# Kernel tuning notes

Measured on AMD Instinct MI355X. Metric: run time of the kernel, lower is better.

The kernel has to match this reference:

```python
import jax, jax.numpy as jnp
import numpy as np

MASK_NEG = 1e30


def setup_inputs() -> dict:
    key = jax.random.key(0)
    k_q, k_k, k_m, k_w1, k_w2, k_v = jax.random.split(key, 6)
    B, S, D, A = 32, 2048, 1024, 1024  # batch, seq, feature dim, attn dim
    # Xavier-uniform-like scale for weights
    lim = float(np.sqrt(6.0 / (D + A)))
    query = jax.random.normal(k_q, (B, D), dtype=jnp.float32)
    keys = jax.random.normal(k_k, (B, S, D), dtype=jnp.float32)
    mask = jax.random.randint(k_m, (B, S), 0, 2) > 0  # True = keep
    W1 = jax.random.uniform(k_w1, (A, D), jnp.float32, -lim, lim)
    W2 = jax.random.uniform(k_w2, (A, D), jnp.float32, -lim, lim)
    v = jax.random.uniform(k_v, (A,), jnp.float32, -lim, lim)
    return {"query": query, "keys": keys, "mask": mask, "W1": W1, "W2": W2, "v": v}


def reference(query, keys, mask, W1, W2, v):
    w1_query = jnp.einsum('bd,ad->ba', query, W1)          # (B, A)
    w2_keys = jnp.einsum('bsd,ad->bsa', keys, W2)          # (B, S, A)
    combined = jnp.tanh(w1_query[:, None, :] + w2_keys)    # (B, S, A)
    scores = jnp.einsum('bsa,a->bs', combined, v)          # (B, S)
    # masked softmax: subtract huge constant at masked-out positions
    scores = scores - (~mask).astype(scores.dtype) * MASK_NEG
    return jax.nn.softmax(scores, axis=-1)
```

## Files before the change

kernel.cpp:

```cpp
#include <hip/hip_runtime.h>
#include <hip/hip_bf16.h>
#include <stdint.h>

#define NB 32
#define NS 2048
#define ND 1024
#define NA 1024
#define MASK_NEG 1e30f

#define BM 256
#define BN 256
#define BK 64
#define NTILES 64

typedef __attribute__((ext_vector_type(4))) float f32x4;
typedef __attribute__((ext_vector_type(8))) __bf16 bf16x8;

__device__ __forceinline__ void glds16(const void* g, void* l) {
  __builtin_amdgcn_global_load_lds(
      (const __attribute__((address_space(1))) uint32_t*)g,
      (__attribute__((address_space(3))) uint32_t*)(uintptr_t)l, 16, 0, 0);
}

__global__ void zero_f32(float* __restrict__ p, int n) {
  int i = blockIdx.x * 256 + threadIdx.x;
  if (i < n) p[i] = 0.f;
}

__global__ __launch_bounds__(256) void cvt_bf16(const float* __restrict__ in,
                                                __bf16* __restrict__ out, int n8) {
  long i = blockIdx.x * 256 + threadIdx.x;
  const long stride = (long)gridDim.x * 256;
  for (; i < n8; i += stride) {
    f32x4 a = ((const f32x4*)in)[2 * i];
    f32x4 b = ((const f32x4*)in)[2 * i + 1];
    bf16x8 o;
#pragma unroll
    for (int j = 0; j < 4; ++j) { o[j] = (__bf16)a[j]; o[4 + j] = (__bf16)b[j]; }
    ((bf16x8*)out)[i] = o;
  }
}

__global__ __launch_bounds__(256) void w1q_kernel(const float* __restrict__ q,
                                                  const float* __restrict__ W1,
                                                  float* __restrict__ w1q) {
  const int b = blockIdx.x;
  const int a0 = blockIdx.y * 64;
  const int t = threadIdx.x;
  const int al = t >> 2;
  const int part = t & 3;
  const float* wrow = W1 + (size_t)(a0 + al) * ND + part * 256;
  const float* qrow = q + (size_t)b * ND + part * 256;
  float sum = 0.f;
#pragma unroll 8
  for (int i = 0; i < 256; i += 4) {
    float4 w = *reinterpret_cast<const float4*>(wrow + i);
    float4 x = *reinterpret_cast<const float4*>(qrow + i);
    sum += w.x * x.x + w.y * x.y + w.z * x.z + w.w * x.w;
  }
  __shared__ float red[256];
  red[t] = sum;
  __syncthreads();
  if (t < 64) {
    w1q[(size_t)b * NA + a0 + t] = red[t * 4] + red[t * 4 + 1] + red[t * 4 + 2] + red[t * 4 + 3];
  }
}

__global__ __launch_bounds__(512, 1) void score_gemm8(
    const __bf16* __restrict__ keysb, const __bf16* __restrict__ W2b,
    const float* __restrict__ w1q, const float* __restrict__ vvec,
    float* __restrict__ scores) {
  __shared__ __bf16 ldsA[6][128 * BK];
  __shared__ __bf16 ldsB[4][128 * BK];

  const int t = threadIdx.x;
  const int bs0 = blockIdx.x * BM;
  const int b = bs0 >> 11;
  const int lane = t & 63;
  const int wid = t >> 6;
  const int wr = wid >> 2;
  const int wc = wid & 3;
  const int lrow = lane & 15;
  const int ko = lane >> 4;

  const int srow = lane >> 3;
  const int scol = (lane & 7) ^ srow;
  const size_t aoffT = (size_t)(bs0 + wid * 16 + srow) * ND + scol * 8;
  const size_t boffT = (size_t)(wid * 16 + srow) * ND + scol * 8;

  const int sl0 = ko ^ (lrow & 7);
  const int sl1 = (4 + ko) ^ (lrow & 7);

#define STAGE_A(T, H)                                                           \
  do {                                                                          \
    if ((T) < NTILES) {                                                         \
      const unsigned slot_ = (2u * (unsigned)(T) + (unsigned)(H)) % 6u;         \
      char* d_ = (char*)ldsA + (slot_ << 14) + wid * 2048;                      \
      const size_t g_ = aoffT + (size_t)((H)*128) * ND + (size_t)(((T)&15) * BK); \
      glds16(keysb + g_, d_);                                                   \
      glds16(keysb + g_ + (size_t)8 * ND, d_ + 1024);                           \
    }                                                                           \
  } while (0)

#define STAGE_B(T, H)                                                           \
  do {                                                                          \
    if ((T) < NTILES) {                                                         \
      const unsigned slot_ = (2u * (unsigned)(T) + (unsigned)(H)) % 4u;         \
      char* d_ = (char*)ldsB + (slot_ << 14) + wid * 2048;                      \
      const size_t g_ = boffT + (size_t)(((T) >> 4) * 256 + (H)*128) * ND +     \
                        (size_t)(((T)&15) * BK);                                \
      glds16(W2b + g_, d_);                                                     \
      glds16(W2b + g_ + (size_t)8 * ND, d_ + 1024);                             \
    }                                                                           \
  } while (0)

#define SB __builtin_amdgcn_sched_barrier(0)
#define P1 __builtin_amdgcn_s_setprio(1)
#define P0 __builtin_amdgcn_s_setprio(0)
#define BAR __builtin_amdgcn_s_barrier()

#define PHASE(TL, M_, N_, STAGE_STMT, WM)                                       \
  do {                                                                          \
    STAGE_STMT;                                                                 \
    if ((N_) == 0) {                                                            \
      const char* Ab_ =                                                         \
          (const char*)ldsA + (((2u * (unsigned)(TL) + (unsigned)wr) % 6u) << 14); \
      _Pragma("unroll") for (int mi = 0; mi < 4; ++mi) {                        \
        const int ra_ = (((M_)*4 + mi) * 16 + lrow) * 128;                      \
        af[mi][0] = *reinterpret_cast<const bf16x8*>(Ab_ + ra_ + sl0 * 16);     \
        af[mi][1] = *reinterpret_cast<const bf16x8*>(Ab_ + ra_ + sl1 * 16);     \
      }                                                                         \
    }                                                                           \
    {                                                                           \
      const char* Bb_ =                                                         \
          (const char*)ldsB + (((2u * (unsigned)(TL) + (unsigned)(wc >> 1)) % 4u) << 14); \
      _Pragma("unroll") for (int nq = 0; nq < 2; ++nq) {                        \
        const int rb_ = (((wc & 1) * 4 + (N_)*2 + nq) * 16 + lrow) * 128;       \
        bfr[nq][0] = *reinterpret_cast<const bf16x8*>(Bb_ + rb_ + sl0 * 16);    \
        bfr[nq][1] = *reinterpret_cast<const bf16x8*>(Bb_ + rb_ + sl1 * 16);    \
      }                                                                         \
    }                                                                           \
    BAR;                                                                        \
    asm volatile("s_waitcnt lgkmcnt(0)");                                       \
    SB;                                                                         \
    P1;                                                                         \
    _Pragma("unroll") for (int mi = 0; mi < 4; ++mi)                            \
        _Pragma("unroll") for (int nq = 0; nq < 2; ++nq) {                      \
      acc[(M_)*4 + mi][(N_)*2 + nq] = __builtin_amdgcn_mfma_f32_16x16x32_bf16(  \
          af[mi][0], bfr[nq][0], acc[(M_)*4 + mi][(N_)*2 + nq], 0, 0, 0);       \
      acc[(M_)*4 + mi][(N_)*2 + nq] = __builtin_amdgcn_mfma_f32_16x16x32_bf16(  \
          af[mi][1], bfr[nq][1], acc[(M_)*4 + mi][(N_)*2 + nq], 0, 0, 0);       \
    }                                                                           \
    P0;                                                                         \
    if (WM) {                                                                   \
      if (it != 31) { asm volatile("s_waitcnt vmcnt(4)"); }                     \
      else { asm volatile("s_waitcnt vmcnt(0)"); }                              \
      SB;                                                                       \
    }                                                                           \
    BAR;                                                                        \
  } while (0)

  f32x4 acc[8][4];
#pragma unroll
  for (int mi = 0; mi < 8; ++mi)
#pragma unroll
    for (int ni = 0; ni < 4; ++ni) acc[mi][ni] = f32x4{0.f, 0.f, 0.f, 0.f};

  bf16x8 af[4][2], bfr[2][2];

  STAGE_A(0, 0);
  STAGE_A(0, 1);
  STAGE_A(1, 0);
  STAGE_A(1, 1);
  STAGE_B(0, 0);
  STAGE_B(0, 1);
  __syncthreads();

  for (int it = 0; it < 32; ++it) {
    const int t0 = 2 * it, t1 = 2 * it + 1;
    PHASE(t0, 0, 0, STAGE_B(t1, 0), 0);
    PHASE(t0, 0, 1, STAGE_B(t1, 1), 0);
    PHASE(t0, 1, 0, STAGE_A(t0 + 2, 0), 0);
    PHASE(t0, 1, 1, STAGE_A(t0 + 2, 1), 1);
    PHASE(t1, 0, 0, STAGE_B(t0 + 2, 0), 0);
    PHASE(t1, 0, 1, { STAGE_B(t0 + 2, 1); STAGE_A(t1 + 2, 0); }, 0);
    PHASE(t1, 1, 0, STAGE_A(t1 + 2, 1), 0);
    PHASE(t1, 1, 1, {}, 1);

    if ((it & 7) == 7) {
      const int a0 = (it >> 3) * BN;
      float w1v[4], vv[4];
#pragma unroll
      for (int ni = 0; ni < 4; ++ni) {
        const int a = a0 + wc * 64 + ni * 16 + lrow;
        w1v[ni] = w1q[(size_t)b * NA + a];
        vv[ni] = vvec[a];
      }
#pragma unroll
      for (int mi = 0; mi < 8; ++mi)
#pragma unroll
        for (int r = 0; r < 4; ++r) {
          float p = 0.f;
#pragma unroll
          for (int ni = 0; ni < 4; ++ni) {
            const float x = acc[mi][ni][r] + w1v[ni];
            const float e = __expf(2.f * x);
            p += (1.f - 2.f * __builtin_amdgcn_rcpf(e + 1.f)) * vv[ni];
          }
          p += __shfl_xor(p, 1);
          p += __shfl_xor(p, 2);
          p += __shfl_xor(p, 4);
          p += __shfl_xor(p, 8);
          if (lrow == 0)
            atomicAdd(&scores[bs0 + wr * 128 + mi * 16 + ko * 4 + r], p);
        }
#pragma unroll
      for (int mi = 0; mi < 8; ++mi)
#pragma unroll
        for (int ni = 0; ni < 4; ++ni) acc[mi][ni] = f32x4{0.f, 0.f, 0.f, 0.f};
    }
  }

#undef STAGE_A
#undef STAGE_B
#undef PHASE
#undef SB
#undef P1
#undef P0
#undef BAR
}

__global__ __launch_bounds__(256) void softmax_kernel(const float* __restrict__ scores,
                                                      const int* __restrict__ mask,
                                                      float* __restrict__ out) {
  const int b = blockIdx.x;
  const int t = threadIdx.x;
  float sc[8];
  float mx = -3.4e38f;
#pragma unroll
  for (int j = 0; j < 8; ++j) {
    int i = t + j * 256;
    float s = scores[b * NS + i];
    if (mask[b * NS + i] == 0) s -= MASK_NEG;
    sc[j] = s;
    mx = fmaxf(mx, s);
  }
#pragma unroll
  for (int off = 1; off < 64; off <<= 1) mx = fmaxf(mx, __shfl_xor(mx, off));
  __shared__ float redm[4];
  __shared__ float reds[4];
  if ((t & 63) == 0) redm[t >> 6] = mx;
  __syncthreads();
  mx = fmaxf(fmaxf(redm[0], redm[1]), fmaxf(redm[2], redm[3]));
  float e[8];
  float sum = 0.f;
#pragma unroll
  for (int j = 0; j < 8; ++j) {
    e[j] = __expf(sc[j] - mx);
    sum += e[j];
  }
#pragma unroll
  for (int off = 1; off < 64; off <<= 1) sum += __shfl_xor(sum, off);
  if ((t & 63) == 0) reds[t >> 6] = sum;
  __syncthreads();
  sum = reds[0] + reds[1] + reds[2] + reds[3];
  float inv = 1.f / sum;
#pragma unroll
  for (int j = 0; j < 8; ++j) out[b * NS + t + j * 256] = e[j] * inv;
}

extern "C" void kernel_launch(void* const* d_in, const int* in_sizes, int n_in,
                              void* d_out, int out_size, void* d_ws, size_t ws_size,
                              hipStream_t stream) {
  const float* q = (const float*)d_in[0];
  const float* keysf = (const float*)d_in[1];
  const int* mask = (const int*)d_in[2];
  const float* W1 = (const float*)d_in[3];
  const float* W2f = (const float*)d_in[4];
  const float* v = (const float*)d_in[5];
  float* out = (float*)d_out;

  float* scores = (float*)d_ws;
  float* w1q = scores + NB * NS;
  __bf16* W2b = (__bf16*)(w1q + NB * NA);
  __bf16* keysb = (__bf16*)((char*)W2b + (size_t)NA * ND * 2);

  zero_f32<<<NB * NS / 256, 256, 0, stream>>>(scores, NB * NS);
  cvt_bf16<<<512, 256, 0, stream>>>(W2f, W2b, NA * ND / 8);
  cvt_bf16<<<2048, 256, 0, stream>>>(keysf, keysb, (int)((size_t)NB * NS * ND / 8));
  w1q_kernel<<<dim3(NB, NA / 64), 256, 0, stream>>>(q, W1, w1q);
  score_gemm8<<<NB * NS / BM, 512, 0, stream>>>(keysb, W2b, w1q, v, scores);
  softmax_kernel<<<NB, 256, 0, stream>>>(scores, mask, out);
}
```

Measured before the change: 257.5 us.

## Fuse keys fp32-to-bf16 conversion into score GEMM first pass

Removes the separate keys conversion kernel. During the first A-column block the GEMM loads fp32 keys into registers, converts them to bf16, writes them to LDS and also stores the bf16 copy to global. Later column blocks then read that copy with direct-to-LDS loads. This avoids a full extra write-and-read pass over keys, but the first 16 tiles now use a register path with full vmcnt waits, which may stall the pipeline there.

```diff
diff --git a/kernel.cpp b/kernel.cpp
--- a/kernel.cpp
+++ b/kernel.cpp
@@ -67,7 +67,8 @@
 }
 
 __global__ __launch_bounds__(512, 1) void score_gemm8(
-    const __bf16* __restrict__ keysb, const __bf16* __restrict__ W2b,
+    const float* __restrict__ keysf, __bf16* __restrict__ keysb,
+    const __bf16* __restrict__ W2b,
     const float* __restrict__ w1q, const float* __restrict__ vvec,
     float* __restrict__ scores) {
   __shared__ __bf16 ldsA[6][128 * BK];
@@ -85,28 +86,56 @@
 
   const int srow = lane >> 3;
   const int scol = (lane & 7) ^ srow;
-  const size_t aoffT = (size_t)(bs0 + wid * 16 + srow) * ND + scol * 8;
   const size_t boffT = (size_t)(wid * 16 + srow) * ND + scol * 8;
 
   const int sl0 = ko ^ (lrow & 7);
   const int sl1 = (4 + ko) ^ (lrow & 7);
 
-#define STAGE_A(T, H)                                                           \
+  f32x4 la[4];
+
+#define ALOAD(T, H)                                                             \
+  do {                                                                          \
+    if ((T) < 16) {                                                             \
+      const float* gp_ = keysf +                                                \
+          (size_t)(bs0 + (H)*128 + wid * 16 + srow) * ND + ((T)&15) * 64 + scol * 8; \
+      la[0] = *reinterpret_cast<const f32x4*>(gp_);                             \
+      la[1] = *reinterpret_cast<const f32x4*>(gp_ + 4);                         \
+      la[2] = *reinterpret_cast<const f32x4*>(gp_ + (size_t)8 * ND);            \
+      la[3] = *reinterpret_cast<const f32x4*>(gp_ + (size_t)8 * ND + 4);        \
+    }                                                                           \
+  } while (0)
+
+#define AWRITE(T, H)                                                            \
   do {                                                                          \
     if ((T) < NTILES) {                                                         \
-      const unsigned slot_ = (2u * (unsigned)(T) + (unsigned)(H)) % 6u;         \
-      char* d_ = (char*)ldsA + (slot_ << 14) + wid * 2048;                      \
-      const size_t g_ = aoffT + (size_t)((H)*128) * ND + (size_t)(((T)&15) * BK); \
-      glds16(keysb + g_, d_);                                                   \
-      glds16(keysb + g_ + (size_t)8 * ND, d_ + 1024);                           \
+      char* du_ = (char*)ldsA + (((2u * (unsigned)(T) + (unsigned)(H)) % 6u) << 14) + \
+                  wid * 2048;                                                   \
+      if ((T) < 16) {                                                           \
+        bf16x8 o0_, o1_;                                                        \
+        _Pragma("unroll") for (int j = 0; j < 4; ++j) {                         \
+          o0_[j] = (__bf16)la[0][j]; o0_[4 + j] = (__bf16)la[1][j];             \
+          o1_[j] = (__bf16)la[2][j]; o1_[4 + j] = (__bf16)la[3][j];             \
+        }                                                                       \
+        *reinterpret_cast<bf16x8*>(du_ + lane * 16) = o0_;                      \
+        *reinterpret_cast<bf16x8*>(du_ + 1024 + lane * 16) = o1_;               \
+        __bf16* gs_ = keysb +                                                   \
+            (size_t)(bs0 + (H)*128 + wid * 16 + srow) * ND + ((T)&15) * 64 + scol * 8; \
+        *reinterpret_cast<bf16x8*>(gs_) = o0_;                                  \
+        *reinterpret_cast<bf16x8*>(gs_ + (size_t)8 * ND) = o1_;                 \
+      } else {                                                                  \
+        const size_t g_ = (size_t)(bs0 + (H)*128 + wid * 16 + srow) * ND +      \
+                          ((T)&15) * 64 + scol * 8;                             \
+        glds16(keysb + g_, du_);                                                \
+        glds16(keysb + g_ + (size_t)8 * ND, du_ + 1024);                        \
+      }                                                                         \
     }                                                                           \
   } while (0)
 
 #define STAGE_B(T, H)                                                           \
   do {                                                                          \
     if ((T) < NTILES) {                                                         \
-      const unsigned slot_ = (2u * (unsigned)(T) + (unsigned)(H)) % 4u;         \
-      char* d_ = (char*)ldsB + (slot_ << 14) + wid * 2048;                      \
+      char* d_ = (char*)ldsB + (((2u * (unsigned)(T) + (unsigned)(H)) % 4u) << 14) + \
+                 wid * 2048;                                                    \
       const size_t g_ = boffT + (size_t)(((T) >> 4) * 256 + (H)*128) * ND +     \
                         (size_t)(((T)&15) * BK);                                \
       glds16(W2b + g_, d_);                                                     \
@@ -119,9 +148,9 @@
 #define P0 __builtin_amdgcn_s_setprio(0)
 #define BAR __builtin_amdgcn_s_barrier()
 
-#define PHASE(TL, M_, N_, STAGE_STMT, WM)                                       \
+#define PHASE(TL, M_, N_, PRE_STMT, WM)                                         \
   do {                                                                          \
-    STAGE_STMT;                                                                 \
+    PRE_STMT;                                                                   \
     if ((N_) == 0) {                                                            \
       const char* Ab_ =                                                         \
           (const char*)ldsA + (((2u * (unsigned)(TL) + (unsigned)wr) % 6u) << 14); \
@@ -153,8 +182,8 @@
     }                                                                           \
     P0;                                                                         \
     if (WM) {                                                                   \
-      if (it != 31) { asm volatile("s_waitcnt vmcnt(4)"); }                     \
-      else { asm volatile("s_waitcnt vmcnt(0)"); }                              \
+      if (it < 7 || it == 31) { asm volatile("s_waitcnt vmcnt(0)"); }           \
+      else { asm volatile("s_waitcnt vmcnt(2)"); }                              \
       SB;                                                                       \
     }                                                                           \
     BAR;                                                                        \
@@ -168,23 +197,23 @@
 
   bf16x8 af[4][2], bfr[2][2];
 
-  STAGE_A(0, 0);
-  STAGE_A(0, 1);
-  STAGE_A(1, 0);
-  STAGE_A(1, 1);
+  ALOAD(0, 0); AWRITE(0, 0);
+  ALOAD(0, 1); AWRITE(0, 1);
+  ALOAD(1, 0); AWRITE(1, 0);
   STAGE_B(0, 0);
   STAGE_B(0, 1);
+  ALOAD(1, 1);
   __syncthreads();
 
   for (int it = 0; it < 32; ++it) {
     const int t0 = 2 * it, t1 = 2 * it + 1;
-    PHASE(t0, 0, 0, STAGE_B(t1, 0), 0);
-    PHASE(t0, 0, 1, STAGE_B(t1, 1), 0);
-    PHASE(t0, 1, 0, STAGE_A(t0 + 2, 0), 0);
-    PHASE(t0, 1, 1, STAGE_A(t0 + 2, 1), 1);
-    PHASE(t1, 0, 0, STAGE_B(t0 + 2, 0), 0);
-    PHASE(t1, 0, 1, { STAGE_B(t0 + 2, 1); STAGE_A(t1 + 2, 0); }, 0);
-    PHASE(t1, 1, 0, STAGE_A(t1 + 2, 1), 0);
+    PHASE(t0, 0, 0, { AWRITE(t1, 1); STAGE_B(t1, 0); ALOAD(t0 + 2, 0); }, 0);
+    PHASE(t0, 0, 1, { STAGE_B(t1, 1); }, 0);
+    PHASE(t0, 1, 0, { AWRITE(t0 + 2, 0); ALOAD(t0 + 2, 1); }, 0);
+    PHASE(t0, 1, 1, {}, 1);
+    PHASE(t1, 0, 0, { AWRITE(t0 + 2, 1); STAGE_B(t0 + 2, 0); ALOAD(t1 + 2, 0); }, 0);
+    PHASE(t1, 0, 1, { STAGE_B(t0 + 2, 1); }, 0);
+    PHASE(t1, 1, 0, { AWRITE(t1 + 2, 0); ALOAD(t1 + 2, 1); }, 0);
     PHASE(t1, 1, 1, {}, 1);
 
     if ((it & 7) == 7) {
@@ -221,7 +250,8 @@
     }
   }
 
-#undef STAGE_A
+#undef ALOAD
+#undef AWRITE
 #undef STAGE_B
 #undef PHASE
 #undef SB
@@ -287,8 +317,7 @@
 
   zero_f32<<<NB * NS / 256, 256, 0, stream>>>(scores, NB * NS);
   cvt_bf16<<<512, 256, 0, stream>>>(W2f, W2b, NA * ND / 8);
-  cvt_bf16<<<2048, 256, 0, stream>>>(keysf, keysb, (int)((size_t)NB * NS * ND / 8));
   w1q_kernel<<<dim3(NB, NA / 64), 256, 0, stream>>>(q, W1, w1q);
-  score_gemm8<<<NB * NS / BM, 512, 0, stream>>>(keysb, W2b, w1q, v, scores);
+  score_gemm8<<<NB * NS / BM, 512, 0, stream>>>(keysf, keysb, W2b, w1q, v, scores);
   softmax_kernel<<<NB, 256, 0, stream>>>(scores, mask, out);
 }
```

After: 250.0 us. -2.9%, faster.
